# Performance work log

Hardware: AMD Instinct MI355X
Metric: run time of the kernel (lower is better)

Reference implementation:

```python
import jax, jax.numpy as jnp
import numpy as np

N_USERS = 100000
N_MOVIES = 50000
N_EDGES = 1000000
IN_CH, HID, OUT = 64, 128, 64


def setup_inputs() -> dict:
    key = jax.random.key(0)
    ks = jax.random.split(key, 8)
    N = N_USERS + N_MOVIES
    return {
        "edge_index": jax.random.randint(ks[0], (2, N_EDGES), 0, N, dtype=jnp.int64)
        if jax.config.jax_enable_x64 else jax.random.randint(ks[0], (2, N_EDGES), 0, N, dtype=jnp.int32),
        "user_emb": jax.random.normal(ks[1], (N_USERS, IN_CH), jnp.float32) * 0.05,
        "movie_emb": jax.random.normal(ks[2], (N_MOVIES, IN_CH), jnp.float32) * 0.05,
        "W1l": jax.random.normal(ks[3], (HID, IN_CH), jnp.float32) * 0.05,
        "b1": jnp.zeros((HID,), jnp.float32),
        "W1r": jax.random.normal(ks[4], (HID, IN_CH), jnp.float32) * 0.05,
        "W2l": jax.random.normal(ks[5], (OUT, HID), jnp.float32) * 0.05,
        "b2": jnp.zeros((OUT,), jnp.float32),
        "W2r": jax.random.normal(ks[6], (OUT, HID), jnp.float32) * 0.05,
    }


def _sage_conv(x, src, dst, Wl, bl, Wr, num_nodes):
    # mean-aggregate neighbor (source) features at destination nodes
    msg_sum = jax.ops.segment_sum(x[src], dst, num_segments=num_nodes)  # [N, d_in]
    deg = jax.ops.segment_sum(jnp.ones(src.shape, x.dtype), dst, num_segments=num_nodes)
    agg = msg_sum / jnp.maximum(deg, 1.0)[:, None]
    # out = lin_l(agg) + lin_r(x); lin_l carries the bias (PyG SAGEConv default)
    return agg @ Wl.T + bl + x @ Wr.T


def reference(edge_index, user_emb, movie_emb, W1l, b1, W1r, W2l, b2, W2r):
    N = user_emb.shape[0] + movie_emb.shape[0]
    src, dst = edge_index[0], edge_index[1]
    x = jnp.concatenate([user_emb, movie_emb], axis=0)  # [N, in_ch]
    x = jax.nn.relu(_sage_conv(x, src, dst, W1l, b1, W1r, N))  # dropout = identity (eval)
    x = _sage_conv(x, src, dst, W2l, b2, W2r, N)
    return x[:N_USERS], x[N_USERS:]
```

## Files before the change

### kernel.cpp

```cpp
#include <hip/hip_runtime.h>

constexpr int N_USERS  = 100000;
constexpr int N_MOVIES = 50000;
constexpr int N_NODES  = N_USERS + N_MOVIES;
constexpr int N_EDGES  = 1000000;
constexpr int CAP      = 32;

typedef __attribute__((ext_vector_type(8))) short bf16x8;
typedef __attribute__((ext_vector_type(8))) unsigned short usx8;
typedef __attribute__((ext_vector_type(4))) float f32x4;

__device__ inline unsigned short bf16_rne(float x) {
    unsigned u = __float_as_uint(x);
    unsigned r = (u + 0x7FFF + ((u >> 16) & 1)) >> 16;
    return (unsigned short)r;
}
__device__ inline float bf16_to_f(short v) {
    return __uint_as_float(((unsigned)(unsigned short)v) << 16);
}

constexpr int ORD_BLKS = (N_EDGES / 8 + 255) / 256;
constexpr int PW_BLKS  = (2 * 128 * 128) / 256;
constexpr int PX_BLKS  = (N_NODES * 8 + 255) / 256;

__global__ __launch_bounds__(256) void prep_fused(const int* __restrict__ ei,
                                                  int* __restrict__ cnt,
                                                  int* __restrict__ ord,
                                                  const float* __restrict__ W1l,
                                                  const float* __restrict__ W1r,
                                                  const float* __restrict__ W2l,
                                                  const float* __restrict__ W2r,
                                                  unsigned short* __restrict__ wb,
                                                  const float* __restrict__ ue,
                                                  const float* __restrict__ me,
                                                  unsigned short* __restrict__ xb) {
    const int ob = blockIdx.x;
    if (ob < ORD_BLKS) {
        int t  = ob * 256 + threadIdx.x;
        int e0 = t * 8;
        if (e0 + 7 < N_EDGES) {
            int4 d0 = *(const int4*)&ei[N_EDGES + e0];
            int4 d1 = *(const int4*)&ei[N_EDGES + e0 + 4];
            int4 o0, o1;
            o0.x = atomicAdd(&cnt[d0.x], 1);
            o0.y = atomicAdd(&cnt[d0.y], 1);
            o0.z = atomicAdd(&cnt[d0.z], 1);
            o0.w = atomicAdd(&cnt[d0.w], 1);
            o1.x = atomicAdd(&cnt[d1.x], 1);
            o1.y = atomicAdd(&cnt[d1.y], 1);
            o1.z = atomicAdd(&cnt[d1.z], 1);
            o1.w = atomicAdd(&cnt[d1.w], 1);
            *(int4*)&ord[e0]     = o0;
            *(int4*)&ord[e0 + 4] = o1;
        } else {
            for (int e = e0; e < N_EDGES; ++e)
                ord[e] = atomicAdd(&cnt[ei[N_EDGES + e]], 1);
        }
        return;
    }
    if (ob < ORD_BLKS + PW_BLKS) {
        int i = (ob - ORD_BLKS) * 256 + threadIdx.x;
        int layer = i >> 14;
        int r     = i & 16383;
        int kc    = r >> 12;
        int oc    = (r >> 9) & 7;
        int lane  = (r >> 3) & 63;
        int j     = r & 7;
        int k = kc * 32 + (lane >> 4) * 8 + j;
        int o = oc * 16 + (lane & 15);
        float v;
        if (layer == 0) v = (k < 64) ? W1l[o * 64 + k] : W1r[o * 64 + (k - 64)];
        else            v = (o < 64) ? W2l[o * 128 + k] : W2r[(o - 64) * 128 + k];
        wb[i] = bf16_rne(v);
        return;
    }
    int i = (ob - ORD_BLKS - PW_BLKS) * 256 + threadIdx.x;
    if (i >= N_NODES * 8) return;
    int n = i >> 3, c = (i & 7) * 8;
    const float* src = (n < N_USERS) ? &ue[(size_t)n * 64 + c]
                                     : &me[(size_t)(n - N_USERS) * 64 + c];
    float4 v0 = *(const float4*)src;
    float4 v1 = *(const float4*)(src + 4);
    usx8 r;
    r[0] = bf16_rne(v0.x); r[1] = bf16_rne(v0.y);
    r[2] = bf16_rne(v0.z); r[3] = bf16_rne(v0.w);
    r[4] = bf16_rne(v1.x); r[5] = bf16_rne(v1.y);
    r[6] = bf16_rne(v1.z); r[7] = bf16_rne(v1.w);
    *(usx8*)&xb[(size_t)n * 64 + c] = r;
}

__global__ __launch_bounds__(256) void csr_scatter(const int* __restrict__ ei,
                                                   const int* __restrict__ ord,
                                                   int* __restrict__ srclist) {
    int t  = blockIdx.x * 256 + threadIdx.x;
    int e0 = t * 4;
    if (e0 + 3 < N_EDGES) {
        int4 s = *(const int4*)&ei[e0];
        int4 d = *(const int4*)&ei[N_EDGES + e0];
        int4 o = *(const int4*)&ord[e0];
        if (o.x < CAP) srclist[(d.x << 5) + o.x] = s.x;
        if (o.y < CAP) srclist[(d.y << 5) + o.y] = s.y;
        if (o.z < CAP) srclist[(d.z << 5) + o.z] = s.z;
        if (o.w < CAP) srclist[(d.w << 5) + o.w] = s.w;
    } else {
        for (int e = e0; e < N_EDGES; ++e) {
            int o = ord[e];
            if (o < CAP) srclist[(ei[N_EDGES + e] << 5) + o] = ei[e];
        }
    }
}

__global__ __launch_bounds__(256) void gather1(const int* __restrict__ cnt,
                                               const int* __restrict__ srclist,
                                               const unsigned short* __restrict__ xb,
                                               unsigned short* __restrict__ aggb) {
    int gid = blockIdx.x * 256 + threadIdx.x;
    int n = gid >> 3, l = gid & 7;
    if (n >= N_NODES) return;
    int deg = cnt[n];
    int m = min(deg, CAP);
    float acc[8] = {};
    for (int i = 0; i < m; ++i) {
        int a = srclist[(n << 5) + i];
        bf16x8 v = *(const bf16x8*)&xb[(size_t)a * 64 + l * 8];
#pragma unroll
        for (int j = 0; j < 8; ++j) acc[j] += bf16_to_f(v[j]);
    }
    float inv = 1.0f / fmaxf((float)deg, 1.0f);
    usx8 r;
#pragma unroll
    for (int j = 0; j < 8; ++j) r[j] = bf16_rne(acc[j] * inv);
    *(usx8*)&aggb[(size_t)n * 64 + l * 8] = r;
}

__global__ __launch_bounds__(256) void gather2_final(const int* __restrict__ cnt,
                                                     const int* __restrict__ srclist,
                                                     const unsigned short* __restrict__ zb,
                                                     const unsigned short* __restrict__ wfb,
                                                     float* __restrict__ out) {
    int gid = blockIdx.x * 256 + threadIdx.x;
    int n = gid >> 3, l = gid & 7;
    if (n >= N_NODES) return;
    int deg = cnt[n];
    int m = min(deg, CAP);
    float acc[8] = {};
    for (int i = 0; i < m; ++i) {
        int a = srclist[(n << 5) + i];
        bf16x8 v = *(const bf16x8*)&zb[(size_t)a * 64 + l * 8];
#pragma unroll
        for (int j = 0; j < 8; ++j) acc[j] += bf16_to_f(v[j]);
    }
    float inv = 1.0f / fmaxf((float)deg, 1.0f);
    bf16x8 wv = *(const bf16x8*)&wfb[(size_t)n * 64 + l * 8];
    float4 r0, r1;
    r0.x = acc[0] * inv + bf16_to_f(wv[0]);
    r0.y = acc[1] * inv + bf16_to_f(wv[1]);
    r0.z = acc[2] * inv + bf16_to_f(wv[2]);
    r0.w = acc[3] * inv + bf16_to_f(wv[3]);
    r1.x = acc[4] * inv + bf16_to_f(wv[4]);
    r1.y = acc[5] * inv + bf16_to_f(wv[5]);
    r1.z = acc[6] * inv + bf16_to_f(wv[6]);
    r1.w = acc[7] * inv + bf16_to_f(wv[7]);
    *(float4*)&out[(size_t)n * 64 + l * 8]     = r0;
    *(float4*)&out[(size_t)n * 64 + l * 8 + 4] = r1;
}

__global__ __launch_bounds__(256) void gemm_fused(const unsigned short* __restrict__ aggb,
                                                  const unsigned short* __restrict__ xb,
                                                  const unsigned short* __restrict__ wb,
                                                  const float* __restrict__ b1,
                                                  const float* __restrict__ b2,
                                                  unsigned short* __restrict__ zb,
                                                  unsigned short* __restrict__ wfb) {
    __shared__ unsigned short hs[128][136];
    const int tid  = threadIdx.x;
    const int w    = tid >> 6;
    const int lane = tid & 63;
    const int n0   = blockIdx.x * 128;
    const int nw   = n0 + w * 32;
    const int lr   = lane & 15;
    const int lg   = lane >> 4;

    {
        f32x4 acc[2][8] = {};
        for (int kc = 0; kc < 4; ++kc) {
            const int k0 = kc * 32 + lg * 8;
            bf16x8 a[2];
#pragma unroll
            for (int f = 0; f < 2; ++f) {
                int node = nw + f * 16 + lr;
                bf16x8 z = {};
                a[f] = z;
                if (node < N_NODES) {
                    const unsigned short* ap = (k0 < 64)
                        ? &aggb[(size_t)node * 64 + k0]
                        : &xb[(size_t)node * 64 + (k0 - 64)];
                    a[f] = *(const bf16x8*)ap;
                }
            }
#pragma unroll
            for (int oc = 0; oc < 8; ++oc) {
                size_t widx = ((size_t)((kc * 8 + oc) * 64 + lane)) * 8;
                bf16x8 wfrag = *(const bf16x8*)&wb[widx];
#pragma unroll
                for (int f = 0; f < 2; ++f)
                    acc[f][oc] = __builtin_amdgcn_mfma_f32_16x16x32_bf16(a[f], wfrag, acc[f][oc], 0, 0, 0);
            }
        }
#pragma unroll
        for (int f = 0; f < 2; ++f) {
#pragma unroll
            for (int oc = 0; oc < 8; ++oc) {
                int col = oc * 16 + lr;
                float b = b1[col];
#pragma unroll
                for (int i = 0; i < 4; ++i) {
                    int rowl = w * 32 + f * 16 + lg * 4 + i;
                    hs[rowl][col] = bf16_rne(fmaxf(acc[f][oc][i] + b, 0.f));
                }
            }
        }
    }
    __syncthreads();

    {
        f32x4 acc[2][8] = {};
        for (int kc = 0; kc < 4; ++kc) {
            const int k0 = kc * 32 + lg * 8;
            bf16x8 a[2];
#pragma unroll
            for (int f = 0; f < 2; ++f) {
                int rowl = w * 32 + f * 16 + lr;
                a[f] = *(const bf16x8*)&hs[rowl][k0];
            }
#pragma unroll
            for (int oc = 0; oc < 8; ++oc) {
                size_t widx = ((size_t)(2048 + (kc * 8 + oc) * 64 + lane)) * 8;
                bf16x8 wfrag = *(const bf16x8*)&wb[widx];
#pragma unroll
                for (int f = 0; f < 2; ++f)
                    acc[f][oc] = __builtin_amdgcn_mfma_f32_16x16x32_bf16(a[f], wfrag, acc[f][oc], 0, 0, 0);
            }
        }
#pragma unroll
        for (int f = 0; f < 2; ++f) {
#pragma unroll
            for (int oc = 0; oc < 8; ++oc) {
                int col = oc * 16 + lr;
                float badd = (oc < 4) ? 0.f : b2[col - 64];
#pragma unroll
                for (int i = 0; i < 4; ++i) {
                    int row = nw + f * 16 + lg * 4 + i;
                    if (row < N_NODES) {
                        unsigned short v = bf16_rne(acc[f][oc][i] + badd);
                        if (oc < 4) zb[(size_t)row * 64 + col] = v;
                        else        wfb[(size_t)row * 64 + (col - 64)] = v;
                    }
                }
            }
        }
    }
}

extern "C" void kernel_launch(void* const* d_in, const int* in_sizes, int n_in,
                              void* d_out, int out_size, void* d_ws, size_t ws_size,
                              hipStream_t stream) {
    const int*   ei  = (const int*)d_in[0];
    const float* ue  = (const float*)d_in[1];
    const float* me  = (const float*)d_in[2];
    const float* W1l = (const float*)d_in[3];
    const float* b1  = (const float*)d_in[4];
    const float* W1r = (const float*)d_in[5];
    const float* W2l = (const float*)d_in[6];
    const float* b2  = (const float*)d_in[7];
    const float* W2r = (const float*)d_in[8];
    float* out = (float*)d_out;

    char* p = (char*)d_ws;
    int* srclist = (int*)p;                   p += (size_t)N_NODES * CAP * 4;
    int* cnt     = (int*)p;                   p += ((N_NODES * 4) + 255) / 256 * 256;
    int* ord     = (int*)p;                   p += (size_t)N_EDGES * 4;
    unsigned short* wb  = (unsigned short*)p; p += 2 * 128 * 128 * 2;
    unsigned short* xb  = (unsigned short*)p; p += (size_t)N_NODES * 64 * 2;
    unsigned short* zb  = (unsigned short*)p; p += (size_t)N_NODES * 64 * 2;
    unsigned short* wfb = (unsigned short*)p; p += (size_t)N_NODES * 64 * 2;
    unsigned short* aggb = (unsigned short*)out;

    hipMemsetAsync(cnt, 0, N_NODES * sizeof(int), stream);
    prep_fused<<<ORD_BLKS + PW_BLKS + PX_BLKS, 256, 0, stream>>>(
        ei, cnt, ord, W1l, W1r, W2l, W2r, wb, ue, me, xb);
    csr_scatter<<<(N_EDGES / 4 + 255) / 256, 256, 0, stream>>>(ei, ord, srclist);

    int gblocks = (N_NODES * 8 + 255) / 256;
    int mblocks = (N_NODES + 127) / 128;

    gather1<<<gblocks, 256, 0, stream>>>(cnt, srclist, xb, aggb);
    gemm_fused<<<mblocks, 256, 0, stream>>>(aggb, xb, wb, b1, b2, zb, wfb);
    gather2_final<<<gblocks, 256, 0, stream>>>(cnt, srclist, zb, wfb, out);
}
```

Measured before the change: 176.9 us.

## Split degree counters into two halves and stage GEMM weights in LDS

Edge degree counting now spreads atomics over two counter arrays, by even and odd edge position, each filling its own 16-slot half of the 32-slot neighbour list. This is meant to reduce atomic contention on the same address. The gather kernels walk both halves and use the summed degree. The fused GEMM also copies each layer's bf16 weight fragments into shared memory once per block instead of reading them from global memory for every MFMA. This adds 32 KB of LDS per block, which may lower occupancy, and neighbours can be dropped when one half overflows 16 while the other has room.

```diff
diff --git a/kernel.cpp b/kernel.cpp
--- a/kernel.cpp
+++ b/kernel.cpp
@@ -24,7 +24,8 @@
 constexpr int PX_BLKS  = (N_NODES * 8 + 255) / 256;
 
 __global__ __launch_bounds__(256) void prep_fused(const int* __restrict__ ei,
-                                                  int* __restrict__ cnt,
+                                                  int* __restrict__ cnt0,
+                                                  int* __restrict__ cnt1,
                                                   int* __restrict__ ord,
                                                   const float* __restrict__ W1l,
                                                   const float* __restrict__ W1r,
@@ -41,20 +42,32 @@
         if (e0 + 7 < N_EDGES) {
             int4 d0 = *(const int4*)&ei[N_EDGES + e0];
             int4 d1 = *(const int4*)&ei[N_EDGES + e0 + 4];
-            int4 o0, o1;
-            o0.x = atomicAdd(&cnt[d0.x], 1);
-            o0.y = atomicAdd(&cnt[d0.y], 1);
-            o0.z = atomicAdd(&cnt[d0.z], 1);
-            o0.w = atomicAdd(&cnt[d0.w], 1);
-            o1.x = atomicAdd(&cnt[d1.x], 1);
-            o1.y = atomicAdd(&cnt[d1.y], 1);
-            o1.z = atomicAdd(&cnt[d1.z], 1);
-            o1.w = atomicAdd(&cnt[d1.w], 1);
-            *(int4*)&ord[e0]     = o0;
-            *(int4*)&ord[e0 + 4] = o1;
+            int o[8];
+            o[0] = atomicAdd(&cnt0[d0.x], 1);
+            o[1] = atomicAdd(&cnt1[d0.y], 1);
+            o[2] = atomicAdd(&cnt0[d0.z], 1);
+            o[3] = atomicAdd(&cnt1[d0.w], 1);
+            o[4] = atomicAdd(&cnt0[d1.x], 1);
+            o[5] = atomicAdd(&cnt1[d1.y], 1);
+            o[6] = atomicAdd(&cnt0[d1.z], 1);
+            o[7] = atomicAdd(&cnt1[d1.w], 1);
+            int4 s0, s1;
+            s0.x = (o[0] < 16) ? o[0]      : -1;
+            s0.y = (o[1] < 16) ? o[1] + 16 : -1;
+            s0.z = (o[2] < 16) ? o[2]      : -1;
+            s0.w = (o[3] < 16) ? o[3] + 16 : -1;
+            s1.x = (o[4] < 16) ? o[4]      : -1;
+            s1.y = (o[5] < 16) ? o[5] + 16 : -1;
+            s1.z = (o[6] < 16) ? o[6]      : -1;
+            s1.w = (o[7] < 16) ? o[7] + 16 : -1;
+            *(int4*)&ord[e0]     = s0;
+            *(int4*)&ord[e0 + 4] = s1;
         } else {
-            for (int e = e0; e < N_EDGES; ++e)
-                ord[e] = atomicAdd(&cnt[ei[N_EDGES + e]], 1);
+            for (int e = e0; e < N_EDGES; ++e) {
+                int d = ei[N_EDGES + e];
+                int o = (e & 1) ? atomicAdd(&cnt1[d], 1) : atomicAdd(&cnt0[d], 1);
+                ord[e] = (o < 16) ? o + (e & 1) * 16 : -1;
+            }
         }
         return;
     }
@@ -98,42 +111,50 @@
         int4 s = *(const int4*)&ei[e0];
         int4 d = *(const int4*)&ei[N_EDGES + e0];
         int4 o = *(const int4*)&ord[e0];
-        if (o.x < CAP) srclist[(d.x << 5) + o.x] = s.x;
-        if (o.y < CAP) srclist[(d.y << 5) + o.y] = s.y;
-        if (o.z < CAP) srclist[(d.z << 5) + o.z] = s.z;
-        if (o.w < CAP) srclist[(d.w << 5) + o.w] = s.w;
+        if (o.x >= 0) srclist[(d.x << 5) + o.x] = s.x;
+        if (o.y >= 0) srclist[(d.y << 5) + o.y] = s.y;
+        if (o.z >= 0) srclist[(d.z << 5) + o.z] = s.z;
+        if (o.w >= 0) srclist[(d.w << 5) + o.w] = s.w;
     } else {
         for (int e = e0; e < N_EDGES; ++e) {
             int o = ord[e];
-            if (o < CAP) srclist[(ei[N_EDGES + e] << 5) + o] = ei[e];
-        }
-    }
-}
-
-__global__ __launch_bounds__(256) void gather1(const int* __restrict__ cnt,
+            if (o >= 0) srclist[(ei[N_EDGES + e] << 5) + o] = ei[e];
+        }
+    }
+}
+
+__global__ __launch_bounds__(256) void gather1(const int* __restrict__ cnt0,
+                                               const int* __restrict__ cnt1,
                                                const int* __restrict__ srclist,
                                                const unsigned short* __restrict__ xb,
                                                unsigned short* __restrict__ aggb) {
     int gid = blockIdx.x * 256 + threadIdx.x;
     int n = gid >> 3, l = gid & 7;
     if (n >= N_NODES) return;
-    int deg = cnt[n];
-    int m = min(deg, CAP);
+    int c0 = cnt0[n], c1 = cnt1[n];
+    int m0 = min(c0, 16), m1 = min(c1, 16);
     float acc[8] = {};
-    for (int i = 0; i < m; ++i) {
+    for (int i = 0; i < m0; ++i) {
         int a = srclist[(n << 5) + i];
         bf16x8 v = *(const bf16x8*)&xb[(size_t)a * 64 + l * 8];
 #pragma unroll
         for (int j = 0; j < 8; ++j) acc[j] += bf16_to_f(v[j]);
     }
-    float inv = 1.0f / fmaxf((float)deg, 1.0f);
+    for (int i = 16; i < 16 + m1; ++i) {
+        int a = srclist[(n << 5) + i];
+        bf16x8 v = *(const bf16x8*)&xb[(size_t)a * 64 + l * 8];
+#pragma unroll
+        for (int j = 0; j < 8; ++j) acc[j] += bf16_to_f(v[j]);
+    }
+    float inv = 1.0f / fmaxf((float)(c0 + c1), 1.0f);
     usx8 r;
 #pragma unroll
     for (int j = 0; j < 8; ++j) r[j] = bf16_rne(acc[j] * inv);
     *(usx8*)&aggb[(size_t)n * 64 + l * 8] = r;
 }
 
-__global__ __launch_bounds__(256) void gather2_final(const int* __restrict__ cnt,
+__global__ __launch_bounds__(256) void gather2_final(const int* __restrict__ cnt0,
+                                                     const int* __restrict__ cnt1,
                                                      const int* __restrict__ srclist,
                                                      const unsigned short* __restrict__ zb,
                                                      const unsigned short* __restrict__ wfb,
@@ -141,16 +162,22 @@
     int gid = blockIdx.x * 256 + threadIdx.x;
     int n = gid >> 3, l = gid & 7;
     if (n >= N_NODES) return;
-    int deg = cnt[n];
-    int m = min(deg, CAP);
+    int c0 = cnt0[n], c1 = cnt1[n];
+    int m0 = min(c0, 16), m1 = min(c1, 16);
     float acc[8] = {};
-    for (int i = 0; i < m; ++i) {
+    for (int i = 0; i < m0; ++i) {
         int a = srclist[(n << 5) + i];
         bf16x8 v = *(const bf16x8*)&zb[(size_t)a * 64 + l * 8];
 #pragma unroll
         for (int j = 0; j < 8; ++j) acc[j] += bf16_to_f(v[j]);
     }
-    float inv = 1.0f / fmaxf((float)deg, 1.0f);
+    for (int i = 16; i < 16 + m1; ++i) {
+        int a = srclist[(n << 5) + i];
+        bf16x8 v = *(const bf16x8*)&zb[(size_t)a * 64 + l * 8];
+#pragma unroll
+        for (int j = 0; j < 8; ++j) acc[j] += bf16_to_f(v[j]);
+    }
+    float inv = 1.0f / fmaxf((float)(c0 + c1), 1.0f);
     bf16x8 wv = *(const bf16x8*)&wfb[(size_t)n * 64 + l * 8];
     float4 r0, r1;
     r0.x = acc[0] * inv + bf16_to_f(wv[0]);
@@ -173,13 +200,20 @@
                                                   unsigned short* __restrict__ zb,
                                                   unsigned short* __restrict__ wfb) {
     __shared__ unsigned short hs[128][136];
+    __shared__ unsigned short wl[16384];
     const int tid  = threadIdx.x;
     const int w    = tid >> 6;
     const int lane = tid & 63;
-    const int n0   = blockIdx.x * 128;
-    const int nw   = n0 + w * 32;
+    const int nw   = blockIdx.x * 128 + w * 32;
     const int lr   = lane & 15;
     const int lg   = lane >> 4;
+
+#pragma unroll
+    for (int r = 0; r < 8; ++r) {
+        int i = r * 256 + tid;
+        *(usx8*)&wl[i * 8] = *(const usx8*)&wb[i * 8];
+    }
+    __syncthreads();
 
     {
         f32x4 acc[2][8] = {};
@@ -200,11 +234,9 @@
             }
 #pragma unroll
             for (int oc = 0; oc < 8; ++oc) {
-                size_t widx = ((size_t)((kc * 8 + oc) * 64 + lane)) * 8;
-                bf16x8 wfrag = *(const bf16x8*)&wb[widx];
-#pragma unroll
-                for (int f = 0; f < 2; ++f)
-                    acc[f][oc] = __builtin_amdgcn_mfma_f32_16x16x32_bf16(a[f], wfrag, acc[f][oc], 0, 0, 0);
+                bf16x8 wfrag = *(const bf16x8*)&wl[((kc * 8 + oc) * 64 + lane) * 8];
+                acc[0][oc] = __builtin_amdgcn_mfma_f32_16x16x32_bf16(a[0], wfrag, acc[0][oc], 0, 0, 0);
+                acc[1][oc] = __builtin_amdgcn_mfma_f32_16x16x32_bf16(a[1], wfrag, acc[1][oc], 0, 0, 0);
             }
         }
 #pragma unroll
@@ -220,6 +252,13 @@
                 }
             }
         }
+    }
+    __syncthreads();
+
+#pragma unroll
+    for (int r = 0; r < 8; ++r) {
+        int i = r * 256 + tid;
+        *(usx8*)&wl[i * 8] = *(const usx8*)&wb[16384 + i * 8];
     }
     __syncthreads();
 
@@ -235,11 +274,9 @@
             }
 #pragma unroll
             for (int oc = 0; oc < 8; ++oc) {
-                size_t widx = ((size_t)(2048 + (kc * 8 + oc) * 64 + lane)) * 8;
-                bf16x8 wfrag = *(const bf16x8*)&wb[widx];
-#pragma unroll
-                for (int f = 0; f < 2; ++f)
-                    acc[f][oc] = __builtin_amdgcn_mfma_f32_16x16x32_bf16(a[f], wfrag, acc[f][oc], 0, 0, 0);
+                bf16x8 wfrag = *(const bf16x8*)&wl[((kc * 8 + oc) * 64 + lane) * 8];
+                acc[0][oc] = __builtin_amdgcn_mfma_f32_16x16x32_bf16(a[0], wfrag, acc[0][oc], 0, 0, 0);
+                acc[1][oc] = __builtin_amdgcn_mfma_f32_16x16x32_bf16(a[1], wfrag, acc[1][oc], 0, 0, 0);
             }
         }
 #pragma unroll
@@ -278,7 +315,8 @@
 
     char* p = (char*)d_ws;
     int* srclist = (int*)p;                   p += (size_t)N_NODES * CAP * 4;
-    int* cnt     = (int*)p;                   p += ((N_NODES * 4) + 255) / 256 * 256;
+    int* cnt0    = (int*)p;                   p += ((2 * N_NODES * 4) + 255) / 256 * 256;
+    int* cnt1    = cnt0 + N_NODES;
     int* ord     = (int*)p;                   p += (size_t)N_EDGES * 4;
     unsigned short* wb  = (unsigned short*)p; p += 2 * 128 * 128 * 2;
     unsigned short* xb  = (unsigned short*)p; p += (size_t)N_NODES * 64 * 2;
@@ -286,15 +324,15 @@
     unsigned short* wfb = (unsigned short*)p; p += (size_t)N_NODES * 64 * 2;
     unsigned short* aggb = (unsigned short*)out;
 
-    hipMemsetAsync(cnt, 0, N_NODES * sizeof(int), stream);
+    hipMemsetAsync(cnt0, 0, 2 * N_NODES * sizeof(int), stream);
     prep_fused<<<ORD_BLKS + PW_BLKS + PX_BLKS, 256, 0, stream>>>(
-        ei, cnt, ord, W1l, W1r, W2l, W2r, wb, ue, me, xb);
+        ei, cnt0, cnt1, ord, W1l, W1r, W2l, W2r, wb, ue, me, xb);
     csr_scatter<<<(N_EDGES / 4 + 255) / 256, 256, 0, stream>>>(ei, ord, srclist);
 
     int gblocks = (N_NODES * 8 + 255) / 256;
     int mblocks = (N_NODES + 127) / 128;
 
-    gather1<<<gblocks, 256, 0, stream>>>(cnt, srclist, xb, aggb);
+    gather1<<<gblocks, 256, 0, stream>>>(cnt0, cnt1, srclist, xb, aggb);
     gemm_fused<<<mblocks, 256, 0, stream>>>(aggb, xb, wb, b1, b2, zb, wfb);
-    gather2_final<<<gblocks, 256, 0, stream>>>(cnt, srclist, zb, wfb, out);
-}
+    gather2_final<<<gblocks, 256, 0, stream>>>(cnt0, cnt1, srclist, zb, wfb, out);
+}
```

Measured after the change: 177.7 us. Within noise of the previous version (+0.5%).

## Fuse layer-1 neighbor gather into the dense GEMM kernel via shared memory

Applied to the files above, without the earlier changes.

Merges the layer-1 mean aggregation with the fused two-stage GEMM. Each 128-node block now gathers its nodes' neighbor features into LDS alongside its own x rows, then runs both MFMA stages from shared memory. This removes one kernel launch and the write and reread of the aggregated buffer through global memory. In exchange, each block does 4 serial gather passes per thread at 1170 blocks, down from about 4.7k gather blocks before, so latency hiding for the irregular gathers may drop. LDS use per block also rises to 40KB.

```diff
diff --git a/kernel.cpp b/kernel.cpp
--- a/kernel.cpp
+++ b/kernel.cpp
@@ -110,27 +110,131 @@
     }
 }
 
-__global__ __launch_bounds__(256) void gather1(const int* __restrict__ cnt,
-                                               const int* __restrict__ srclist,
-                                               const unsigned short* __restrict__ xb,
-                                               unsigned short* __restrict__ aggb) {
-    int gid = blockIdx.x * 256 + threadIdx.x;
-    int n = gid >> 3, l = gid & 7;
-    if (n >= N_NODES) return;
-    int deg = cnt[n];
-    int m = min(deg, CAP);
-    float acc[8] = {};
-    for (int i = 0; i < m; ++i) {
-        int a = srclist[(n << 5) + i];
-        bf16x8 v = *(const bf16x8*)&xb[(size_t)a * 64 + l * 8];
-#pragma unroll
-        for (int j = 0; j < 8; ++j) acc[j] += bf16_to_f(v[j]);
-    }
-    float inv = 1.0f / fmaxf((float)deg, 1.0f);
-    usx8 r;
-#pragma unroll
-    for (int j = 0; j < 8; ++j) r[j] = bf16_rne(acc[j] * inv);
-    *(usx8*)&aggb[(size_t)n * 64 + l * 8] = r;
+__global__ __launch_bounds__(256) void fused_l1(const int* __restrict__ cnt,
+                                                const int* __restrict__ srclist,
+                                                const unsigned short* __restrict__ xb,
+                                                const unsigned short* __restrict__ wb,
+                                                const float* __restrict__ b1,
+                                                const float* __restrict__ b2,
+                                                unsigned short* __restrict__ zb,
+                                                unsigned short* __restrict__ wfb) {
+    __shared__ unsigned short U[20480];
+    const int tid  = threadIdx.x;
+    const int w    = tid >> 6;
+    const int lane = tid & 63;
+    const int n0   = blockIdx.x * 128;
+    const int lr   = lane & 15;
+    const int lg   = lane >> 4;
+    const int XOFF = 10240;
+
+#pragma unroll
+    for (int r = 0; r < 4; ++r) {
+        int c = r * 256 + tid;
+        int row = c >> 3, off = (c & 7) * 8;
+        usx8 v = {};
+        int node = n0 + row;
+        if (node < N_NODES) v = *(const usx8*)&xb[(size_t)node * 64 + off];
+        *(usx8*)&U[XOFF + row * 80 + off] = v;
+    }
+
+#pragma unroll
+    for (int p = 0; p < 4; ++p) {
+        int nl = p * 32 + (tid >> 3);
+        int l  = tid & 7;
+        int node = n0 + nl;
+        float acc[8] = {};
+        int deg = 0;
+        if (node < N_NODES) {
+            deg = cnt[node];
+            int m = min(deg, CAP);
+            for (int i = 0; i < m; ++i) {
+                int a = srclist[(node << 5) + i];
+                bf16x8 v = *(const bf16x8*)&xb[(size_t)a * 64 + l * 8];
+#pragma unroll
+                for (int j = 0; j < 8; ++j) acc[j] += bf16_to_f(v[j]);
+            }
+        }
+        float inv = 1.0f / fmaxf((float)deg, 1.0f);
+        usx8 r;
+#pragma unroll
+        for (int j = 0; j < 8; ++j) r[j] = bf16_rne(acc[j] * inv);
+        *(usx8*)&U[nl * 80 + l * 8] = r;
+    }
+    __syncthreads();
+
+    f32x4 acc[2][8] = {};
+    for (int kc = 0; kc < 4; ++kc) {
+        const int k0 = kc * 32 + lg * 8;
+        bf16x8 a[2];
+#pragma unroll
+        for (int f = 0; f < 2; ++f) {
+            int rowl = w * 32 + f * 16 + lr;
+            const unsigned short* ap = (k0 < 64)
+                ? &U[rowl * 80 + k0]
+                : &U[XOFF + rowl * 80 + (k0 - 64)];
+            a[f] = *(const bf16x8*)ap;
+        }
+#pragma unroll
+        for (int oc = 0; oc < 8; ++oc) {
+            size_t widx = ((size_t)((kc * 8 + oc) * 64 + lane)) * 8;
+            bf16x8 wfrag = *(const bf16x8*)&wb[widx];
+            acc[0][oc] = __builtin_amdgcn_mfma_f32_16x16x32_bf16(a[0], wfrag, acc[0][oc], 0, 0, 0);
+            acc[1][oc] = __builtin_amdgcn_mfma_f32_16x16x32_bf16(a[1], wfrag, acc[1][oc], 0, 0, 0);
+        }
+    }
+    __syncthreads();
+
+#pragma unroll
+    for (int f = 0; f < 2; ++f) {
+#pragma unroll
+        for (int oc = 0; oc < 8; ++oc) {
+            int col = oc * 16 + lr;
+            float b = b1[col];
+#pragma unroll
+            for (int i = 0; i < 4; ++i) {
+                int rowl = w * 32 + f * 16 + lg * 4 + i;
+                U[rowl * 136 + col] = bf16_rne(fmaxf(acc[f][oc][i] + b, 0.f));
+            }
+        }
+    }
+    __syncthreads();
+
+    {
+        f32x4 acc2[2][8] = {};
+        for (int kc = 0; kc < 4; ++kc) {
+            const int k0 = kc * 32 + lg * 8;
+            bf16x8 a[2];
+#pragma unroll
+            for (int f = 0; f < 2; ++f) {
+                int rowl = w * 32 + f * 16 + lr;
+                a[f] = *(const bf16x8*)&U[rowl * 136 + k0];
+            }
+#pragma unroll
+            for (int oc = 0; oc < 8; ++oc) {
+                size_t widx = ((size_t)(2048 + (kc * 8 + oc) * 64 + lane)) * 8;
+                bf16x8 wfrag = *(const bf16x8*)&wb[widx];
+                acc2[0][oc] = __builtin_amdgcn_mfma_f32_16x16x32_bf16(a[0], wfrag, acc2[0][oc], 0, 0, 0);
+                acc2[1][oc] = __builtin_amdgcn_mfma_f32_16x16x32_bf16(a[1], wfrag, acc2[1][oc], 0, 0, 0);
+            }
+        }
+#pragma unroll
+        for (int f = 0; f < 2; ++f) {
+#pragma unroll
+            for (int oc = 0; oc < 8; ++oc) {
+                int col = oc * 16 + lr;
+                float badd = (oc < 4) ? 0.f : b2[col - 64];
+#pragma unroll
+                for (int i = 0; i < 4; ++i) {
+                    int row = n0 + w * 32 + f * 16 + lg * 4 + i;
+                    if (row < N_NODES) {
+                        unsigned short v = bf16_rne(acc2[f][oc][i] + badd);
+                        if (oc < 4) zb[(size_t)row * 64 + col] = v;
+                        else        wfb[(size_t)row * 64 + (col - 64)] = v;
+                    }
+                }
+            }
+        }
+    }
 }
 
 __global__ __launch_bounds__(256) void gather2_final(const int* __restrict__ cnt,
@@ -165,103 +269,6 @@
     *(float4*)&out[(size_t)n * 64 + l * 8 + 4] = r1;
 }
 
-__global__ __launch_bounds__(256) void gemm_fused(const unsigned short* __restrict__ aggb,
-                                                  const unsigned short* __restrict__ xb,
-                                                  const unsigned short* __restrict__ wb,
-                                                  const float* __restrict__ b1,
-                                                  const float* __restrict__ b2,
-                                                  unsigned short* __restrict__ zb,
-                                                  unsigned short* __restrict__ wfb) {
-    __shared__ unsigned short hs[128][136];
-    const int tid  = threadIdx.x;
-    const int w    = tid >> 6;
-    const int lane = tid & 63;
-    const int n0   = blockIdx.x * 128;
-    const int nw   = n0 + w * 32;
-    const int lr   = lane & 15;
-    const int lg   = lane >> 4;
-
-    {
-        f32x4 acc[2][8] = {};
-        for (int kc = 0; kc < 4; ++kc) {
-            const int k0 = kc * 32 + lg * 8;
-            bf16x8 a[2];
-#pragma unroll
-            for (int f = 0; f < 2; ++f) {
-                int node = nw + f * 16 + lr;
-                bf16x8 z = {};
-                a[f] = z;
-                if (node < N_NODES) {
-                    const unsigned short* ap = (k0 < 64)
-                        ? &aggb[(size_t)node * 64 + k0]
-                        : &xb[(size_t)node * 64 + (k0 - 64)];
-                    a[f] = *(const bf16x8*)ap;
-                }
-            }
-#pragma unroll
-            for (int oc = 0; oc < 8; ++oc) {
-                size_t widx = ((size_t)((kc * 8 + oc) * 64 + lane)) * 8;
-                bf16x8 wfrag = *(const bf16x8*)&wb[widx];
-#pragma unroll
-                for (int f = 0; f < 2; ++f)
-                    acc[f][oc] = __builtin_amdgcn_mfma_f32_16x16x32_bf16(a[f], wfrag, acc[f][oc], 0, 0, 0);
-            }
-        }
-#pragma unroll
-        for (int f = 0; f < 2; ++f) {
-#pragma unroll
-            for (int oc = 0; oc < 8; ++oc) {
-                int col = oc * 16 + lr;
-                float b = b1[col];
-#pragma unroll
-                for (int i = 0; i < 4; ++i) {
-                    int rowl = w * 32 + f * 16 + lg * 4 + i;
-                    hs[rowl][col] = bf16_rne(fmaxf(acc[f][oc][i] + b, 0.f));
-                }
-            }
-        }
-    }
-    __syncthreads();
-
-    {
-        f32x4 acc[2][8] = {};
-        for (int kc = 0; kc < 4; ++kc) {
-            const int k0 = kc * 32 + lg * 8;
-            bf16x8 a[2];
-#pragma unroll
-            for (int f = 0; f < 2; ++f) {
-                int rowl = w * 32 + f * 16 + lr;
-                a[f] = *(const bf16x8*)&hs[rowl][k0];
-            }
-#pragma unroll
-            for (int oc = 0; oc < 8; ++oc) {
-                size_t widx = ((size_t)(2048 + (kc * 8 + oc) * 64 + lane)) * 8;
-                bf16x8 wfrag = *(const bf16x8*)&wb[widx];
-#pragma unroll
-                for (int f = 0; f < 2; ++f)
-                    acc[f][oc] = __builtin_amdgcn_mfma_f32_16x16x32_bf16(a[f], wfrag, acc[f][oc], 0, 0, 0);
-            }
-        }
-#pragma unroll
-        for (int f = 0; f < 2; ++f) {
-#pragma unroll
-            for (int oc = 0; oc < 8; ++oc) {
-                int col = oc * 16 + lr;
-                float badd = (oc < 4) ? 0.f : b2[col - 64];
-#pragma unroll
-                for (int i = 0; i < 4; ++i) {
-                    int row = nw + f * 16 + lg * 4 + i;
-                    if (row < N_NODES) {
-                        unsigned short v = bf16_rne(acc[f][oc][i] + badd);
-                        if (oc < 4) zb[(size_t)row * 64 + col] = v;
-                        else        wfb[(size_t)row * 64 + (col - 64)] = v;
-                    }
-                }
-            }
-        }
-    }
-}
-
 extern "C" void kernel_launch(void* const* d_in, const int* in_sizes, int n_in,
                               void* d_out, int out_size, void* d_ws, size_t ws_size,
                               hipStream_t stream) {
@@ -284,17 +291,15 @@
     unsigned short* xb  = (unsigned short*)p; p += (size_t)N_NODES * 64 * 2;
     unsigned short* zb  = (unsigned short*)p; p += (size_t)N_NODES * 64 * 2;
     unsigned short* wfb = (unsigned short*)p; p += (size_t)N_NODES * 64 * 2;
-    unsigned short* aggb = (unsigned short*)out;
 
     hipMemsetAsync(cnt, 0, N_NODES * sizeof(int), stream);
     prep_fused<<<ORD_BLKS + PW_BLKS + PX_BLKS, 256, 0, stream>>>(
         ei, cnt, ord, W1l, W1r, W2l, W2r, wb, ue, me, xb);
     csr_scatter<<<(N_EDGES / 4 + 255) / 256, 256, 0, stream>>>(ei, ord, srclist);
 
+    int mblocks = (N_NODES + 127) / 128;
+    fused_l1<<<mblocks, 256, 0, stream>>>(cnt, srclist, xb, wb, b1, b2, zb, wfb);
+
     int gblocks = (N_NODES * 8 + 255) / 256;
-    int mblocks = (N_NODES + 127) / 128;
-
-    gather1<<<gblocks, 256, 0, stream>>>(cnt, srclist, xb, aggb);
-    gemm_fused<<<mblocks, 256, 0, stream>>>(aggb, xb, wb, b1, b2, zb, wfb);
     gather2_final<<<gblocks, 256, 0, stream>>>(cnt, srclist, zb, wfb, out);
 }
```

After: 210.3 us. 18.9% more time.
